# Optimization experiments

Hardware: AMD Instinct MI355X
Metric: run time of the kernel (lower is better)

The kernel has to match this reference:

```python
import jax, jax.numpy as jnp
import numpy as np

N = 100000      # nodes
E = 800000      # edges
D = 96          # feature dim (feats_per_node == layer_1_feats == layer_2_feats)
NEG_SLOPE = 0.01  # torch.nn.LeakyReLU default


def setup_inputs() -> dict:
    key = jax.random.key(0)
    kx, ks, kd, k1, k2, k3, k4 = jax.random.split(key, 7)
    # ensure every node appears at least once as a source row so e_rowsum > 0
    src = jnp.concatenate([jnp.arange(N, dtype=jnp.int64),
                           jax.random.randint(ks, (E - N,), 0, N, dtype=jnp.int64)])
    dst = jax.random.randint(kd, (E,), 0, N, dtype=jnp.int64)
    edge_index = jnp.stack([src, dst])  # [2, E]
    x = jax.random.normal(kx, (N, D), dtype=jnp.float32)
    # xavier-normal-like params, scaled down to keep exp() well-behaved
    W1 = jax.random.normal(k1, (D, D), dtype=jnp.float32) * 0.1
    a1 = jax.random.normal(k2, (1, 2 * D), dtype=jnp.float32) * 0.1
    W2 = jax.random.normal(k3, (D, D), dtype=jnp.float32) * 0.1
    a2 = jax.random.normal(k4, (1, 2 * D), dtype=jnp.float32) * 0.1
    return {"edge_index": edge_index, "x": x, "W1": W1, "a1": a1, "W2": W2, "a2": a2}


def _gat_layer(h_in, W, a, src, dst):
    h = h_in @ W                                   # [N, D]
    d = h.shape[1]
    # a @ cat(h[src], h[dst]) without materializing the concat:
    s = h[src] @ a[0, :d] + h[dst] @ a[0, d:]      # [E]
    e = jnp.exp(-jax.nn.leaky_relu(s, NEG_SLOPE))  # [E]
    n = h.shape[0]
    rowsum = jax.ops.segment_sum(e, src, num_segments=n)               # spmm(edge, e, ones)
    h_prime = jax.ops.segment_sum(e[:, None] * h[dst], src, num_segments=n)  # spmm(edge, e, h)
    return h_prime / rowsum[:, None]


def reference(edge_index, x, W1, a1, W2, a2):
    src, dst = edge_index[0], edge_index[1]
    h = _gat_layer(x, W1, a1, src, dst)
    h = _gat_layer(h, W2, a2, src, dst)
    return jax.nn.relu(h)
```

## Files before the change

### kernel.cpp

```cpp
#include <hip/hip_runtime.h>
#include <hip/hip_bf16.h>

#define NN 100000
#define NE 800000
#define DIM 96
#define NEG_SLOPE 0.01f
#define SCAN_BLOCKS ((NN + 255) / 256)
#define EDGE_BLOCKS ((NE + 255) / 256)
#define CONV_BLOCKS ((2 * DIM * DIM + 255) / 256)
#define AGG_BLOCKS  ((NN / 2 + 3) / 4)

typedef short bf16x8 __attribute__((ext_vector_type(8)));
typedef float f32x4  __attribute__((ext_vector_type(4)));
typedef float f32x2  __attribute__((ext_vector_type(2)));

__device__ __forceinline__ unsigned short f32_to_bf16_rne(float f) {
    unsigned int u = __float_as_uint(f);
    unsigned int r = (u + 0x7FFFu + ((u >> 16) & 1u)) >> 16;
    return (unsigned short)r;
}
__device__ __forceinline__ float bf16lo_to_f32(unsigned int u) { return __uint_as_float(u << 16); }
__device__ __forceinline__ float bf16hi_to_f32(unsigned int u) { return __uint_as_float(u & 0xFFFF0000u); }

__device__ __forceinline__ int   rdlane_i(int v, int l)   { return __builtin_amdgcn_readlane(v, l); }
__device__ __forceinline__ float rdlane_f(float v, int l) {
    return __uint_as_float((unsigned int)__builtin_amdgcn_readlane((int)__float_as_uint(v), l));
}


__global__ __launch_bounds__(256) void hist_conv_kernel(const int* __restrict__ src, int* __restrict__ deg,
                                                        const float* __restrict__ W1, unsigned short* __restrict__ Wt1,
                                                        const float* __restrict__ W2, unsigned short* __restrict__ Wt2) {
    if (blockIdx.x < EDGE_BLOCKS) {
        int e = blockIdx.x * 256 + threadIdx.x;
        if (e < NE) atomicAdd(&deg[src[e]], 1);
    } else {
        int idx = (blockIdx.x - EDGE_BLOCKS) * 256 + threadIdx.x;
        if (idx < DIM * DIM) {
            int n = idx / DIM, k = idx % DIM;
            Wt1[n * DIM + k] = f32_to_bf16_rne(W1[k * DIM + n]);
        } else if (idx < 2 * DIM * DIM) {
            int j = idx - DIM * DIM;
            int n = j / DIM, k = j % DIM;
            Wt2[n * DIM + k] = f32_to_bf16_rne(W2[k * DIM + n]);
        }
    }
}

__global__ __launch_bounds__(256) void partial_kernel(const int* __restrict__ deg, int* __restrict__ blocksum) {
    __shared__ int lds[4];
    int idx = blockIdx.x * 256 + threadIdx.x;
    int v = (idx < NN) ? deg[idx] : 0;
    for (int off = 32; off > 0; off >>= 1) v += __shfl_down(v, off);
    int wave = threadIdx.x >> 6;
    int lane = threadIdx.x & 63;
    if (lane == 0) lds[wave] = v;
    __syncthreads();
    if (threadIdx.x == 0) blocksum[blockIdx.x] = lds[0] + lds[1] + lds[2] + lds[3];
}

__global__ __launch_bounds__(512) void scan_partials_kernel(const int* __restrict__ blocksum, int* __restrict__ blockoff) {
    __shared__ int lds[512];
    int i = threadIdx.x;
    int v = (i < SCAN_BLOCKS) ? blocksum[i] : 0;
    lds[i] = v;
    __syncthreads();
    for (int off = 1; off < 512; off <<= 1) {
        int t = (i >= off) ? lds[i - off] : 0;
        __syncthreads();
        lds[i] += t;
        __syncthreads();
    }
    if (i < SCAN_BLOCKS) blockoff[i] = lds[i] - v;
}

__global__ __launch_bounds__(256) void rowptr_kernel(const int* __restrict__ deg, const int* __restrict__ blockoff,
                                                     int* __restrict__ row_ptr, int* __restrict__ cursor) {
    __shared__ int lds[256];
    int i = threadIdx.x;
    int idx = blockIdx.x * 256 + i;
    int v = (idx < NN) ? deg[idx] : 0;
    lds[i] = v;
    __syncthreads();
    for (int off = 1; off < 256; off <<= 1) {
        int t = (i >= off) ? lds[i - off] : 0;
        __syncthreads();
        lds[i] += t;
        __syncthreads();
    }
    if (idx < NN) {
        int r = blockoff[blockIdx.x] + lds[i] - v;
        row_ptr[idx] = r;
        cursor[idx]  = r;
    }
    if (idx == 0) row_ptr[NN] = NE;
}

__global__ __launch_bounds__(256) void fill_kernel(const int* __restrict__ src, const int* __restrict__ dst,
                                                   int* __restrict__ cursor, int* __restrict__ dst_perm) {
    int e = blockIdx.x * 256 + threadIdx.x;
    if (e < NE) {
        int s = src[e];
        int pos = atomicAdd(&cursor[s], 1);
        dst_perm[pos] = dst[e];
    }
}


template <bool A_BF16>
__global__ __launch_bounds__(256) void gemm_mfma_kernel(const void* __restrict__ A_,
                                                        const unsigned short* __restrict__ Wt,
                                                        const float* __restrict__ avec,
                                                        unsigned short* __restrict__ Hout,
                                                        float* __restrict__ ssrc, float* __restrict__ sdst,
                                                        int n) {
    const int wave = threadIdx.x >> 6;
    const int lane = threadIdx.x & 63;
    const int quad = lane >> 4;
    const int l16  = lane & 15;
    const int R0   = blockIdx.x * 64 + wave * 16;

    bf16x8 bfr[6][3];
#pragma unroll
    for (int nt = 0; nt < 6; nt++) {
        const unsigned short* wrow = Wt + (size_t)(nt * 16 + l16) * DIM;
#pragma unroll
        for (int kc = 0; kc < 3; kc++) bfr[nt][kc] = *(const bf16x8*)(wrow + kc * 32 + quad * 8);
    }

    int arow = R0 + l16;
    if (arow >= n) arow = n - 1;
    bf16x8 afr[3];
    if (A_BF16) {
        const unsigned short* ap = (const unsigned short*)A_ + (size_t)arow * DIM;
#pragma unroll
        for (int kc = 0; kc < 3; kc++) afr[kc] = *(const bf16x8*)(ap + kc * 32 + quad * 8);
    } else {
        const float* ap = (const float*)A_ + (size_t)arow * DIM;
#pragma unroll
        for (int kc = 0; kc < 3; kc++) {
            float4 lo = *(const float4*)(ap + kc * 32 + quad * 8);
            float4 hi = *(const float4*)(ap + kc * 32 + quad * 8 + 4);
            union { bf16x8 v; unsigned short u[8]; } t;
            t.u[0] = f32_to_bf16_rne(lo.x); t.u[1] = f32_to_bf16_rne(lo.y);
            t.u[2] = f32_to_bf16_rne(lo.z); t.u[3] = f32_to_bf16_rne(lo.w);
            t.u[4] = f32_to_bf16_rne(hi.x); t.u[5] = f32_to_bf16_rne(hi.y);
            t.u[6] = f32_to_bf16_rne(hi.z); t.u[7] = f32_to_bf16_rne(hi.w);
            afr[kc] = t.v;
        }
    }

    f32x4 acc[6];
#pragma unroll
    for (int nt = 0; nt < 6; nt++) acc[nt] = (f32x4){0.f, 0.f, 0.f, 0.f};
#pragma unroll
    for (int kc = 0; kc < 3; kc++)
#pragma unroll
        for (int nt = 0; nt < 6; nt++)
            acc[nt] = __builtin_amdgcn_mfma_f32_16x16x32_bf16(afr[kc], bfr[nt][kc], acc[nt], 0, 0, 0);

    float as_[6], ad_[6];
#pragma unroll
    for (int nt = 0; nt < 6; nt++) {
        as_[nt] = avec[nt * 16 + l16];
        ad_[nt] = avec[96 + nt * 16 + l16];
    }
    float ps[4], pd[4];
#pragma unroll
    for (int r = 0; r < 4; r++) {
        float s = 0.f, d = 0.f;
#pragma unroll
        for (int nt = 0; nt < 6; nt++) {
            s = fmaf(acc[nt][r], as_[nt], s);
            d = fmaf(acc[nt][r], ad_[nt], d);
        }
        ps[r] = s; pd[r] = d;
    }
#pragma unroll
    for (int m = 1; m < 16; m <<= 1) {
#pragma unroll
        for (int r = 0; r < 4; r++) {
            ps[r] += __shfl_xor(ps[r], m);
            pd[r] += __shfl_xor(pd[r], m);
        }
    }
    {
        float psel = (l16 == 0) ? ps[0] : (l16 == 1) ? ps[1] : (l16 == 2) ? ps[2] : ps[3];
        float dsel = (l16 == 8) ? pd[0] : (l16 == 9) ? pd[1] : (l16 == 10) ? pd[2] : pd[3];
        int rs = R0 + quad * 4 + l16;
        int rd = R0 + quad * 4 + (l16 - 8);
        if (l16 < 4 && rs < n) ssrc[rs] = psel;
        if (l16 >= 8 && l16 < 12 && rd < n) sdst[rd] = dsel;
    }

#pragma unroll
    for (int r = 0; r < 4; r++) {
        int orow = R0 + quad * 4 + r;
        if (orow < n) {
            unsigned short* hrow = Hout + (size_t)orow * DIM;
#pragma unroll
            for (int nt = 0; nt < 6; nt++) hrow[nt * 16 + l16] = f32_to_bf16_rne(acc[nt][r]);
        }
    }
}


template <bool RELU, bool OUT_BF16>
__global__ __launch_bounds__(256) void agg_kernel(const unsigned short* __restrict__ h,
                                                  const float* __restrict__ ssrc,
                                                  const float* __restrict__ sdst,
                                                  const int* __restrict__ row_ptr,
                                                  const int* __restrict__ dst_perm,
                                                  void* __restrict__ out) {
    int gid  = blockIdx.x * 256 + threadIdx.x;
    int wid  = gid >> 6;
    int lane = threadIdx.x & 63;
    int n0   = wid * 2;
    if (n0 >= NN) return;
    int n1 = n0 + 1;

    int s0  = row_ptr[n0];
    int m01 = row_ptr[n0 + 1];
    int e1  = row_ptr[n0 + 2];
    float ss = ssrc[n0 + ((lane >> 3) & 1)];
    const bool act = lane < 48;
    const int  li8 = lane & 7;

    float a00 = 0.f, a01 = 0.f, w0 = 0.f;
    float a10 = 0.f, a11 = 0.f, w1 = 0.f;

    int p0 = s0, p1 = m01;
    while (p0 < m01 || p1 < e1) {
        const int c0 = m01 - p0;
        const int c1 = e1 - p1;
        int idx = (lane < 8) ? min(p0 + lane, m01 - 1) : min(p1 + li8, e1 - 1);
        int dv  = dst_perm[idx];

        bool valid = (lane < 8) ? (lane < c0) : ((lane < 16) && (li8 < c1));
        float sv = 0.f;
        if (valid) sv = sdst[dv];

        unsigned int u0[8], u1[8];
#pragma unroll
        for (int i = 0; i < 8; i++) {
            int d0i = rdlane_i(dv, i);
            int d1i = rdlane_i(dv, 8 + i);
            if (act) {
                u0[i] = ((const unsigned int*)(h + (size_t)d0i * DIM))[lane];
                u1[i] = ((const unsigned int*)(h + (size_t)d1i * DIM))[lane];
            }
        }

        float wl = 0.f;
        if (valid) {
            float s  = ss + sv;
            float lr = s > 0.f ? s : NEG_SLOPE * s;
            wl = __expf(-lr);
        }

#pragma unroll
        for (int i = 0; i < 8; i++) {
            float wa = rdlane_f(wl, i);
            float wb = rdlane_f(wl, 8 + i);
            w0 += wa; w1 += wb;
            if (act) {
                a00 = fmaf(wa, bf16lo_to_f32(u0[i]), a00);
                a01 = fmaf(wa, bf16hi_to_f32(u0[i]), a01);
                a10 = fmaf(wb, bf16lo_to_f32(u1[i]), a10);
                a11 = fmaf(wb, bf16hi_to_f32(u1[i]), a11);
            }
        }
        p0 += 8; p1 += 8;
    }

    float inv0 = 1.f / w0;
    float inv1 = 1.f / w1;
    float r00 = a00 * inv0, r01 = a01 * inv0;
    float r10 = a10 * inv1, r11 = a11 * inv1;
    if (RELU) {
        r00 = fmaxf(r00, 0.f); r01 = fmaxf(r01, 0.f);
        r10 = fmaxf(r10, 0.f); r11 = fmaxf(r11, 0.f);
    }
    if (act) {
        if (OUT_BF16) {
            unsigned int pk0 = (unsigned int)f32_to_bf16_rne(r00) | ((unsigned int)f32_to_bf16_rne(r01) << 16);
            unsigned int pk1 = (unsigned int)f32_to_bf16_rne(r10) | ((unsigned int)f32_to_bf16_rne(r11) << 16);
            ((unsigned int*)out)[(size_t)n0 * 48 + lane] = pk0;
            ((unsigned int*)out)[(size_t)n1 * 48 + lane] = pk1;
        } else {
            f32x2 v0; v0.x = r00; v0.y = r01;
            f32x2 v1; v1.x = r10; v1.y = r11;
            __builtin_nontemporal_store(v0, &((f32x2*)out)[(size_t)n0 * 48 + lane]);
            __builtin_nontemporal_store(v1, &((f32x2*)out)[(size_t)n1 * 48 + lane]);
        }
    }
}


extern "C" void kernel_launch(void* const* d_in, const int* in_sizes, int n_in,
                              void* d_out, int out_size, void* d_ws, size_t ws_size,
                              hipStream_t stream) {
    (void)in_sizes; (void)n_in; (void)out_size; (void)ws_size;
    const int*   edge_index = (const int*)d_in[0];
    const float* x  = (const float*)d_in[1];
    const float* W1 = (const float*)d_in[2];
    const float* a1 = (const float*)d_in[3];
    const float* W2 = (const float*)d_in[4];
    const float* a2 = (const float*)d_in[5];
    float* out = (float*)d_out;

    const int* src = edge_index;
    const int* dst = edge_index + NE;

    char* ws = (char*)d_ws;
    size_t off = 0;
    auto alloc = [&](size_t bytes) -> void* {
        void* p = ws + off;
        off += (bytes + 255) & ~(size_t)255;
        return p;
    };
    unsigned short* h1 = (unsigned short*)alloc((size_t)NN * DIM * 2);
    unsigned short* h2 = (unsigned short*)alloc((size_t)NN * DIM * 2);
    float* ssrc      = (float*)alloc((size_t)NN * 4);
    float* sdst      = (float*)alloc((size_t)NN * 4);
    int*   deg       = (int*)alloc((size_t)NN * 4);
    int*   row_ptr   = (int*)alloc((size_t)(NN + 1) * 4);
    int*   cursor    = (int*)alloc((size_t)NN * 4);
    int*   dst_perm  = (int*)alloc((size_t)NE * 4);
    int*   blocksum  = (int*)alloc((size_t)SCAN_BLOCKS * 4);
    int*   blockoff  = (int*)alloc((size_t)SCAN_BLOCKS * 4);
    unsigned short* Wt1 = (unsigned short*)alloc((size_t)DIM * DIM * 2);
    unsigned short* Wt2 = (unsigned short*)alloc((size_t)DIM * DIM * 2);

    hipMemsetAsync(deg, 0, (size_t)NN * 4, stream);
    hist_conv_kernel<<<EDGE_BLOCKS + CONV_BLOCKS, 256, 0, stream>>>(src, deg, W1, Wt1, W2, Wt2);
    partial_kernel<<<SCAN_BLOCKS, 256, 0, stream>>>(deg, blocksum);
    scan_partials_kernel<<<1, 512, 0, stream>>>(blocksum, blockoff);
    rowptr_kernel<<<SCAN_BLOCKS, 256, 0, stream>>>(deg, blockoff, row_ptr, cursor);
    fill_kernel<<<EDGE_BLOCKS, 256, 0, stream>>>(src, dst, cursor, dst_perm);

    int gemm_grid = (NN + 63) / 64;

    gemm_mfma_kernel<false><<<gemm_grid, 256, 0, stream>>>(x, Wt1, a1, h1, ssrc, sdst, NN);
    agg_kernel<false, true><<<AGG_BLOCKS, 256, 0, stream>>>(h1, ssrc, sdst, row_ptr, dst_perm, h2);

    gemm_mfma_kernel<true><<<gemm_grid, 256, 0, stream>>>(h2, Wt2, a2, h1, ssrc, sdst, NN);
    agg_kernel<true, false><<<AGG_BLOCKS, 256, 0, stream>>>(h1, ssrc, sdst, row_ptr, dst_perm, out);
}
```

Baseline: 272.9 us.

## Scatter edges into padded per-node buckets during histogram, compact alongside first GEMM

```diff
diff --git a/kernel.cpp b/kernel.cpp
--- a/kernel.cpp
+++ b/kernel.cpp
@@ -5,9 +5,11 @@
 #define NE 800000
 #define DIM 96
 #define NEG_SLOPE 0.01f
+#define PAD 48
 #define SCAN_BLOCKS ((NN + 255) / 256)
 #define EDGE_BLOCKS ((NE + 255) / 256)
 #define CONV_BLOCKS ((2 * DIM * DIM + 255) / 256)
+#define GEMM_GRID   ((NN + 63) / 64)
 #define AGG_BLOCKS  ((NN / 2 + 3) / 4)
 
 typedef short bf16x8 __attribute__((ext_vector_type(8)));
@@ -28,12 +30,18 @@
 }
 
 
-__global__ __launch_bounds__(256) void hist_conv_kernel(const int* __restrict__ src, int* __restrict__ deg,
-                                                        const float* __restrict__ W1, unsigned short* __restrict__ Wt1,
-                                                        const float* __restrict__ W2, unsigned short* __restrict__ Wt2) {
+__global__ __launch_bounds__(256) void scatter_conv_kernel(const int* __restrict__ src, const int* __restrict__ dst,
+                                                           int* __restrict__ cnt, int* __restrict__ temp,
+                                                           const float* __restrict__ W1, unsigned short* __restrict__ Wt1,
+                                                           const float* __restrict__ W2, unsigned short* __restrict__ Wt2) {
     if (blockIdx.x < EDGE_BLOCKS) {
         int e = blockIdx.x * 256 + threadIdx.x;
-        if (e < NE) atomicAdd(&deg[src[e]], 1);
+        if (e < NE) {
+            int s = src[e];
+            int r = atomicAdd(&cnt[s], 1);
+            r = min(r, PAD - 1);
+            temp[(size_t)s * PAD + r] = dst[e];
+        }
     } else {
         int idx = (blockIdx.x - EDGE_BLOCKS) * 256 + threadIdx.x;
         if (idx < DIM * DIM) {
@@ -47,10 +55,11 @@
     }
 }
 
-__global__ __launch_bounds__(256) void partial_kernel(const int* __restrict__ deg, int* __restrict__ blocksum) {
+
+__global__ __launch_bounds__(256) void partial_kernel(const int* __restrict__ cnt, int* __restrict__ blocksum) {
     __shared__ int lds[4];
     int idx = blockIdx.x * 256 + threadIdx.x;
-    int v = (idx < NN) ? deg[idx] : 0;
+    int v = (idx < NN) ? cnt[idx] : 0;
     for (int off = 32; off > 0; off >>= 1) v += __shfl_down(v, off);
     int wave = threadIdx.x >> 6;
     int lane = threadIdx.x & 63;
@@ -74,12 +83,12 @@
     if (i < SCAN_BLOCKS) blockoff[i] = lds[i] - v;
 }
 
-__global__ __launch_bounds__(256) void rowptr_kernel(const int* __restrict__ deg, const int* __restrict__ blockoff,
-                                                     int* __restrict__ row_ptr, int* __restrict__ cursor) {
+__global__ __launch_bounds__(256) void rowptr_kernel(const int* __restrict__ cnt, const int* __restrict__ blockoff,
+                                                     int* __restrict__ row_ptr) {
     __shared__ int lds[256];
     int i = threadIdx.x;
     int idx = blockIdx.x * 256 + i;
-    int v = (idx < NN) ? deg[idx] : 0;
+    int v = (idx < NN) ? cnt[idx] : 0;
     lds[i] = v;
     __syncthreads();
     for (int off = 1; off < 256; off <<= 1) {
@@ -88,37 +97,23 @@
         lds[i] += t;
         __syncthreads();
     }
-    if (idx < NN) {
-        int r = blockoff[blockIdx.x] + lds[i] - v;
-        row_ptr[idx] = r;
-        cursor[idx]  = r;
-    }
+    if (idx < NN) row_ptr[idx] = blockoff[blockIdx.x] + lds[i] - v;
     if (idx == 0) row_ptr[NN] = NE;
 }
 
-__global__ __launch_bounds__(256) void fill_kernel(const int* __restrict__ src, const int* __restrict__ dst,
-                                                   int* __restrict__ cursor, int* __restrict__ dst_perm) {
-    int e = blockIdx.x * 256 + threadIdx.x;
-    if (e < NE) {
-        int s = src[e];
-        int pos = atomicAdd(&cursor[s], 1);
-        dst_perm[pos] = dst[e];
-    }
-}
-
 
 template <bool A_BF16>
-__global__ __launch_bounds__(256) void gemm_mfma_kernel(const void* __restrict__ A_,
-                                                        const unsigned short* __restrict__ Wt,
-                                                        const float* __restrict__ avec,
-                                                        unsigned short* __restrict__ Hout,
-                                                        float* __restrict__ ssrc, float* __restrict__ sdst,
-                                                        int n) {
+__device__ __forceinline__ void gemm_body(int bid, const void* __restrict__ A_,
+                                          const unsigned short* __restrict__ Wt,
+                                          const float* __restrict__ avec,
+                                          unsigned short* __restrict__ Hout,
+                                          float* __restrict__ ssrc, float* __restrict__ sdst,
+                                          int n) {
     const int wave = threadIdx.x >> 6;
     const int lane = threadIdx.x & 63;
     const int quad = lane >> 4;
     const int l16  = lane & 15;
-    const int R0   = blockIdx.x * 64 + wave * 16;
+    const int R0   = bid * 64 + wave * 16;
 
     bf16x8 bfr[6][3];
 #pragma unroll
@@ -200,6 +195,39 @@
             unsigned short* hrow = Hout + (size_t)orow * DIM;
 #pragma unroll
             for (int nt = 0; nt < 6; nt++) hrow[nt * 16 + l16] = f32_to_bf16_rne(acc[nt][r]);
+        }
+    }
+}
+
+template <bool A_BF16>
+__global__ __launch_bounds__(256) void gemm_mfma_kernel(const void* __restrict__ A_,
+                                                        const unsigned short* __restrict__ Wt,
+                                                        const float* __restrict__ avec,
+                                                        unsigned short* __restrict__ Hout,
+                                                        float* __restrict__ ssrc, float* __restrict__ sdst,
+                                                        int n) {
+    gemm_body<A_BF16>(blockIdx.x, A_, Wt, avec, Hout, ssrc, sdst, n);
+}
+
+
+__global__ __launch_bounds__(256) void gemm1_compact_kernel(const float* __restrict__ x,
+                                                            const unsigned short* __restrict__ Wt1,
+                                                            const float* __restrict__ a1,
+                                                            unsigned short* __restrict__ h1,
+                                                            float* __restrict__ ssrc, float* __restrict__ sdst,
+                                                            const int* __restrict__ cnt,
+                                                            const int* __restrict__ row_ptr,
+                                                            const int* __restrict__ temp,
+                                                            int* __restrict__ dst_perm) {
+    if (blockIdx.x < GEMM_GRID) {
+        gemm_body<false>(blockIdx.x, x, Wt1, a1, h1, ssrc, sdst, NN);
+    } else {
+        int n = (blockIdx.x - GEMM_GRID) * 256 + threadIdx.x;
+        if (n < NN) {
+            int c  = min(cnt[n], PAD);
+            int rp = row_ptr[n];
+            const int* tr = temp + (size_t)n * PAD;
+            for (int i = 0; i < c; i++) dst_perm[rp + i] = tr[i];
         }
     }
 }
@@ -323,27 +351,26 @@
     unsigned short* h2 = (unsigned short*)alloc((size_t)NN * DIM * 2);
     float* ssrc      = (float*)alloc((size_t)NN * 4);
     float* sdst      = (float*)alloc((size_t)NN * 4);
-    int*   deg       = (int*)alloc((size_t)NN * 4);
+    int*   cnt       = (int*)alloc((size_t)NN * 4);
     int*   row_ptr   = (int*)alloc((size_t)(NN + 1) * 4);
-    int*   cursor    = (int*)alloc((size_t)NN * 4);
     int*   dst_perm  = (int*)alloc((size_t)NE * 4);
     int*   blocksum  = (int*)alloc((size_t)SCAN_BLOCKS * 4);
     int*   blockoff  = (int*)alloc((size_t)SCAN_BLOCKS * 4);
     unsigned short* Wt1 = (unsigned short*)alloc((size_t)DIM * DIM * 2);
     unsigned short* Wt2 = (unsigned short*)alloc((size_t)DIM * DIM * 2);
 
-    hipMemsetAsync(deg, 0, (size_t)NN * 4, stream);
-    hist_conv_kernel<<<EDGE_BLOCKS + CONV_BLOCKS, 256, 0, stream>>>(src, deg, W1, Wt1, W2, Wt2);
-    partial_kernel<<<SCAN_BLOCKS, 256, 0, stream>>>(deg, blocksum);
+    int* temp = (int*)h2;
+
+    hipMemsetAsync(cnt, 0, (size_t)NN * 4, stream);
+    scatter_conv_kernel<<<EDGE_BLOCKS + CONV_BLOCKS, 256, 0, stream>>>(src, dst, cnt, temp, W1, Wt1, W2, Wt2);
+    partial_kernel<<<SCAN_BLOCKS, 256, 0, stream>>>(cnt, blocksum);
     scan_partials_kernel<<<1, 512, 0, stream>>>(blocksum, blockoff);
-    rowptr_kernel<<<SCAN_BLOCKS, 256, 0, stream>>>(deg, blockoff, row_ptr, cursor);
-    fill_kernel<<<EDGE_BLOCKS, 256, 0, stream>>>(src, dst, cursor, dst_perm);
-
-    int gemm_grid = (NN + 63) / 64;
-
-    gemm_mfma_kernel<false><<<gemm_grid, 256, 0, stream>>>(x, Wt1, a1, h1, ssrc, sdst, NN);
+    rowptr_kernel<<<SCAN_BLOCKS, 256, 0, stream>>>(cnt, blockoff, row_ptr);
+
+    gemm1_compact_kernel<<<GEMM_GRID + SCAN_BLOCKS, 256, 0, stream>>>(x, Wt1, a1, h1, ssrc, sdst,
+                                                                     cnt, row_ptr, temp, dst_perm);
     agg_kernel<false, true><<<AGG_BLOCKS, 256, 0, stream>>>(h1, ssrc, sdst, row_ptr, dst_perm, h2);
 
-    gemm_mfma_kernel<true><<<gemm_grid, 256, 0, stream>>>(h2, Wt2, a2, h1, ssrc, sdst, NN);
+    gemm_mfma_kernel<true><<<GEMM_GRID, 256, 0, stream>>>(h2, Wt2, a2, h1, ssrc, sdst, NN);
     agg_kernel<true, false><<<AGG_BLOCKS, 256, 0, stream>>>(h1, ssrc, sdst, row_ptr, dst_perm, out);
 }
```

After: 249.8 us. 1.09x faster.
